# Kernel optimization log

Hardware: AMD Instinct MI355X
Metric: run time of the kernel (lower is better)

Reference implementation:

```python
import jax, jax.numpy as jnp
import numpy as np

IN_F = 4096
OUT_F = 4096
THRESH = 0.1

def setup_inputs() -> dict:
    key = jax.random.key(0)
    kx, kw = jax.random.split(key)
    x = jax.random.normal(kx, (4, 2048, IN_F), dtype=jnp.float32)
    weight = jax.random.normal(kw, (OUT_F, IN_F), dtype=jnp.float32) * 0.5
    bias = jnp.zeros((OUT_F,), dtype=jnp.float32)
    return {"x": x, "weight": weight, "bias": bias}

def reference(x, weight, bias):
    # ternary quantization: sign(w) where |w| > 0.1, else 0
    q = jnp.sign(weight) * (jnp.abs(weight) > THRESH).astype(weight.dtype)
    # straight-through estimator: forward uses q, gradient flows to weight
    w_ste = weight + jax.lax.stop_gradient(q - weight)
    # F.linear: x @ w_ste.T + bias
    return jnp.einsum('bsi,oi->bso', x, w_ste) + bias
```

## Files before the change

### kernel.cpp

```cpp
#include <hip/hip_runtime.h>
#include <cstdint>
#include <cstddef>

#define MDIM 8192
#define NDIM 4096
#define KDIM 4096
#define TERN_THRESH 0.1f

typedef unsigned short u16;
typedef __bf16 bf16x8 __attribute__((ext_vector_type(8)));
typedef float f32x4 __attribute__((ext_vector_type(4)));
typedef u16 u16x8 __attribute__((ext_vector_type(8)));


__device__ __forceinline__ u16 f2bf(float f) {
  unsigned u = __float_as_uint(f);
  u += 0x7FFFu + ((u >> 16) & 1u);
  return (u16)(u >> 16);
}

__device__ __forceinline__ u16 tern_bf16(float w) {
  return w > TERN_THRESH ? (u16)0x3F80u : (w < -TERN_THRESH ? (u16)0xBF80u : (u16)0u);
}

__device__ __forceinline__ void load_lds16(const u16* g, u16* s) {
  __builtin_amdgcn_global_load_lds(
      (__attribute__((address_space(1))) void*)(void*)(g),
      (__attribute__((address_space(3))) void*)(void*)(s),
      16, 0, 0);
}


#define XBLOCKS ((MDIM * (size_t)KDIM) / (8 * 256))
#define WBLOCKS ((NDIM * (size_t)KDIM) / (8 * 256))

__global__ __launch_bounds__(256) void cvt_kernel(const float* __restrict__ x,
                                                  u16* __restrict__ xb,
                                                  const float* __restrict__ w,
                                                  u16* __restrict__ qb) {
  size_t b = blockIdx.x;
  if (b < XBLOCKS) {
    size_t i = b * 256 + threadIdx.x;
    const f32x4* x4 = (const f32x4*)x;
    f32x4 a = __builtin_nontemporal_load(&x4[2 * i]);
    f32x4 c = __builtin_nontemporal_load(&x4[2 * i + 1]);
    u16x8 o;
    o[0] = f2bf(a[0]); o[1] = f2bf(a[1]); o[2] = f2bf(a[2]); o[3] = f2bf(a[3]);
    o[4] = f2bf(c[0]); o[5] = f2bf(c[1]); o[6] = f2bf(c[2]); o[7] = f2bf(c[3]);
    ((u16x8*)xb)[i] = o;
  } else {
    size_t i = (b - XBLOCKS) * 256 + threadIdx.x;
    const f32x4* w4 = (const f32x4*)w;
    f32x4 a = __builtin_nontemporal_load(&w4[2 * i]);
    f32x4 c = __builtin_nontemporal_load(&w4[2 * i + 1]);
    u16x8 o;
    o[0] = tern_bf16(a[0]); o[1] = tern_bf16(a[1]); o[2] = tern_bf16(a[2]); o[3] = tern_bf16(a[3]);
    o[4] = tern_bf16(c[0]); o[5] = tern_bf16(c[1]); o[6] = tern_bf16(c[2]); o[7] = tern_bf16(c[3]);
    ((u16x8*)qb)[i] = o;
  }
}


#define NTILE (KDIM / 32)

#define BARRIER() __builtin_amdgcn_s_barrier()
#define FENCE()   asm volatile("" ::: "memory")
#define VMCNT8()  asm volatile("s_waitcnt vmcnt(8)" ::: "memory")

#define MFMA_BLK(I0)                                                         \
  do {                                                                       \
    _Pragma("unroll") for (int _i = 0; _i < 4; ++_i) {                       \
      _Pragma("unroll") for (int _j = 0; _j < 4; ++_j) {                     \
        acc[(I0) + _i][_j] = __builtin_amdgcn_mfma_f32_16x16x32_bf16(        \
            af[_i], bf[_j], acc[(I0) + _i][_j], 0, 0, 0);                    \
      }                                                                      \
    }                                                                        \
  } while (0)

__global__ __launch_bounds__(512, 2) void gemm_tern_kernel(
    const u16* __restrict__ Xb,
    const u16* __restrict__ Qb,
    const float* __restrict__ bias,
    float* __restrict__ C) {
  __shared__ __attribute__((aligned(16))) u16 As[4 * 8192];
  __shared__ __attribute__((aligned(16))) u16 Bs[4 * 8192];

  const int tid  = threadIdx.x;
  const int lane = tid & 63;
  const int wv   = tid >> 6;
  const int wm   = wv >> 2;
  const int wn   = wv & 3;
  const int quad = lane >> 4;
  const int l16  = lane & 15;

  const int orig    = blockIdx.y * 16 + blockIdx.x;
  const int wg      = (orig & 7) * 64 + (orig >> 3);
  const int rowBase = (wg >> 4) * 256;
  const int colBase = (wg & 15) * 256;

  const u16* gA[2];
  const u16* gB[2];
  int sOff[2];
#pragma unroll
  for (int j = 0; j < 2; ++j) {
    int c  = j * 512 + tid;
    int r  = c >> 2;
    int qg = (c & 3) ^ ((r >> 1) & 3);
    gA[j]   = Xb + (size_t)(rowBase + r) * KDIM + qg * 8;
    gB[j]   = Qb + (size_t)(colBase + r) * KDIM + qg * 8;
    sOff[j] = c * 8;
  }

#define STAGE_A(s, kt)                                              \
  do {                                                              \
    load_lds16(gA[0] + (kt), (u16*)As + (s) * 8192 + sOff[0]);      \
    load_lds16(gA[1] + (kt), (u16*)As + (s) * 8192 + sOff[1]);      \
  } while (0)
#define STAGE_B(s, kt)                                              \
  do {                                                              \
    load_lds16(gB[0] + (kt), (u16*)Bs + (s) * 8192 + sOff[0]);      \
    load_lds16(gB[1] + (kt), (u16*)Bs + (s) * 8192 + sOff[1]);      \
  } while (0)

  int ac[8], bc[4];
#pragma unroll
  for (int i = 0; i < 8; ++i) {
    int r = wm * 128 + i * 16 + l16;
    ac[i] = (r * 4 + (quad ^ ((r >> 1) & 3))) * 8;
  }
#pragma unroll
  for (int j = 0; j < 4; ++j) {
    int r = wn * 64 + j * 16 + l16;
    bc[j] = (r * 4 + (quad ^ ((r >> 1) & 3))) * 8;
  }

#define RD_A(d, i, s) d = *(const bf16x8*)((const u16*)As + (s) * 8192 + ac[i])
#define RD_B(d, j, s) d = *(const bf16x8*)((const u16*)Bs + (s) * 8192 + bc[j])

  f32x4 acc[8][4] = {};
  bf16x8 af[4], bf[4];

  STAGE_A(0, 0);  STAGE_B(0, 0);
  STAGE_A(1, 32); STAGE_B(1, 32);
  STAGE_A(2, 64); STAGE_B(2, 64);
  VMCNT8();
  FENCE(); BARRIER(); FENCE();

#define TILE_BODY(S)                                                       \
  do {                                                                     \
    const int kt = (t + 3 < NTILE) ? (t + 3) * 32 : 0;                     \
                                         \
    RD_A(af[0], 0, S); RD_A(af[1], 1, S);                                  \
    RD_A(af[2], 2, S); RD_A(af[3], 3, S);                                  \
    RD_B(bf[0], 0, S); RD_B(bf[1], 1, S);                                  \
    RD_B(bf[2], 2, S); RD_B(bf[3], 3, S);                                  \
    STAGE_A(((S) + 3) & 3, kt);                                            \
    FENCE(); BARRIER(); FENCE();                                           \
    __builtin_amdgcn_s_setprio(1);                                         \
    MFMA_BLK(0);                                                           \
    __builtin_amdgcn_s_setprio(0);                                         \
    FENCE(); BARRIER(); FENCE();                                           \
                                         \
    RD_A(af[0], 4, S); RD_A(af[1], 5, S);                                  \
    RD_A(af[2], 6, S); RD_A(af[3], 7, S);                                  \
    STAGE_B(((S) + 3) & 3, kt);                                            \
    FENCE(); BARRIER(); FENCE();                                           \
    __builtin_amdgcn_s_setprio(1);                                         \
    MFMA_BLK(4);                                                           \
    __builtin_amdgcn_s_setprio(0);                                         \
    VMCNT8();                                                              \
    FENCE(); BARRIER(); FENCE();                                           \
  } while (0)

  int t = 0;
  for (int it = 0; it < NTILE / 4; ++it) {
    TILE_BODY(0); ++t;
    TILE_BODY(1); ++t;
    TILE_BODY(2); ++t;
    TILE_BODY(3); ++t;
  }

  float bv[4];
#pragma unroll
  for (int j = 0; j < 4; ++j) bv[j] = bias[colBase + wn * 64 + j * 16 + l16];

#pragma unroll
  for (int i = 0; i < 8; ++i) {
#pragma unroll
    for (int r = 0; r < 4; ++r) {
      int grow = rowBase + wm * 128 + i * 16 + quad * 4 + r;
      float* crow = C + (size_t)grow * NDIM + colBase + wn * 64 + l16;
#pragma unroll
      for (int j = 0; j < 4; ++j) {
        crow[j * 16] = acc[i][j][r] + bv[j];
      }
    }
  }
}


extern "C" void kernel_launch(void* const* d_in, const int* in_sizes, int n_in,
                              void* d_out, int out_size, void* d_ws, size_t ws_size,
                              hipStream_t stream) {
  const float* x    = (const float*)d_in[0];
  const float* w    = (const float*)d_in[1];
  const float* bias = (const float*)d_in[2];
  float* out = (float*)d_out;

  u16* xb = (u16*)d_ws;
  u16* qb = xb + (size_t)MDIM * KDIM;

  cvt_kernel<<<(unsigned)(XBLOCKS + WBLOCKS), 256, 0, stream>>>(x, xb, w, qb);

  dim3 grid(NDIM / 256, MDIM / 256);
  gemm_tern_kernel<<<grid, 512, 0, stream>>>(xb, qb, bias, out);
}
```

Baseline: 457.0 us.

## Double-buffer MFMA fragments in registers and cut GEMM barriers to one per tile

```diff
diff --git a/kernel.cpp b/kernel.cpp
--- a/kernel.cpp
+++ b/kernel.cpp
@@ -10,6 +10,7 @@
 typedef unsigned short u16;
 typedef __bf16 bf16x8 __attribute__((ext_vector_type(8)));
 typedef float f32x4 __attribute__((ext_vector_type(4)));
+typedef u16 u16x4 __attribute__((ext_vector_type(4)));
 typedef u16 u16x8 __attribute__((ext_vector_type(8)));
 
 
@@ -40,23 +41,27 @@
                                                   u16* __restrict__ qb) {
   size_t b = blockIdx.x;
   if (b < XBLOCKS) {
-    size_t i = b * 256 + threadIdx.x;
+    size_t i0 = b * 512 + threadIdx.x;
+    size_t i1 = i0 + 256;
     const f32x4* x4 = (const f32x4*)x;
-    f32x4 a = __builtin_nontemporal_load(&x4[2 * i]);
-    f32x4 c = __builtin_nontemporal_load(&x4[2 * i + 1]);
-    u16x8 o;
-    o[0] = f2bf(a[0]); o[1] = f2bf(a[1]); o[2] = f2bf(a[2]); o[3] = f2bf(a[3]);
-    o[4] = f2bf(c[0]); o[5] = f2bf(c[1]); o[6] = f2bf(c[2]); o[7] = f2bf(c[3]);
-    ((u16x8*)xb)[i] = o;
+    f32x4 a = __builtin_nontemporal_load(&x4[i0]);
+    f32x4 c = __builtin_nontemporal_load(&x4[i1]);
+    u16x4 oa, oc;
+    oa[0] = f2bf(a[0]); oa[1] = f2bf(a[1]); oa[2] = f2bf(a[2]); oa[3] = f2bf(a[3]);
+    oc[0] = f2bf(c[0]); oc[1] = f2bf(c[1]); oc[2] = f2bf(c[2]); oc[3] = f2bf(c[3]);
+    ((u16x4*)xb)[i0] = oa;
+    ((u16x4*)xb)[i1] = oc;
   } else {
-    size_t i = (b - XBLOCKS) * 256 + threadIdx.x;
+    size_t i0 = (b - XBLOCKS) * 512 + threadIdx.x;
+    size_t i1 = i0 + 256;
     const f32x4* w4 = (const f32x4*)w;
-    f32x4 a = __builtin_nontemporal_load(&w4[2 * i]);
-    f32x4 c = __builtin_nontemporal_load(&w4[2 * i + 1]);
-    u16x8 o;
-    o[0] = tern_bf16(a[0]); o[1] = tern_bf16(a[1]); o[2] = tern_bf16(a[2]); o[3] = tern_bf16(a[3]);
-    o[4] = tern_bf16(c[0]); o[5] = tern_bf16(c[1]); o[6] = tern_bf16(c[2]); o[7] = tern_bf16(c[3]);
-    ((u16x8*)qb)[i] = o;
+    f32x4 a = __builtin_nontemporal_load(&w4[i0]);
+    f32x4 c = __builtin_nontemporal_load(&w4[i1]);
+    u16x4 oa, oc;
+    oa[0] = tern_bf16(a[0]); oa[1] = tern_bf16(a[1]); oa[2] = tern_bf16(a[2]); oa[3] = tern_bf16(a[3]);
+    oc[0] = tern_bf16(c[0]); oc[1] = tern_bf16(c[1]); oc[2] = tern_bf16(c[2]); oc[3] = tern_bf16(c[3]);
+    ((u16x4*)qb)[i0] = oa;
+    ((u16x4*)qb)[i1] = oc;
   }
 }
 
@@ -65,14 +70,14 @@
 
 #define BARRIER() __builtin_amdgcn_s_barrier()
 #define FENCE()   asm volatile("" ::: "memory")
-#define VMCNT8()  asm volatile("s_waitcnt vmcnt(8)" ::: "memory")
-
-#define MFMA_BLK(I0)                                                         \
+#define VMCNT4()  asm volatile("s_waitcnt vmcnt(4)" ::: "memory")
+
+#define MFMA16(AF, BF, I0)                                                   \
   do {                                                                       \
     _Pragma("unroll") for (int _i = 0; _i < 4; ++_i) {                       \
       _Pragma("unroll") for (int _j = 0; _j < 4; ++_j) {                     \
         acc[(I0) + _i][_j] = __builtin_amdgcn_mfma_f32_16x16x32_bf16(        \
-            af[_i], bf[_j], acc[(I0) + _i][_j], 0, 0, 0);                    \
+            AF[_i], BF[_j], acc[(I0) + _i][_j], 0, 0, 0);                    \
       }                                                                      \
     }                                                                        \
   } while (0)
@@ -138,47 +143,51 @@
 #define RD_B(d, j, s) d = *(const bf16x8*)((const u16*)Bs + (s) * 8192 + bc[j])
 
   f32x4 acc[8][4] = {};
-  bf16x8 af[4], bf[4];
+  bf16x8 a0[4], b0[4], a1[4], b1[4], ab[4];
 
   STAGE_A(0, 0);  STAGE_B(0, 0);
   STAGE_A(1, 32); STAGE_B(1, 32);
   STAGE_A(2, 64); STAGE_B(2, 64);
-  VMCNT8();
+  VMCNT4();
   FENCE(); BARRIER(); FENCE();
-
-#define TILE_BODY(S)                                                       \
+  RD_A(a0[0], 0, 0); RD_A(a0[1], 1, 0); RD_A(a0[2], 2, 0); RD_A(a0[3], 3, 0);
+  RD_B(b0[0], 0, 0); RD_B(b0[1], 1, 0); RD_B(b0[2], 2, 0); RD_B(b0[3], 3, 0);
+
+#define TILE(S, AC, BC, AN, BN, PRE)                                       \
   do {                                                                     \
     const int kt = (t + 3 < NTILE) ? (t + 3) * 32 : 0;                     \
-                                         \
-    RD_A(af[0], 0, S); RD_A(af[1], 1, S);                                  \
-    RD_A(af[2], 2, S); RD_A(af[3], 3, S);                                  \
-    RD_B(bf[0], 0, S); RD_B(bf[1], 1, S);                                  \
-    RD_B(bf[2], 2, S); RD_B(bf[3], 3, S);                                  \
+    RD_A(ab[0], 4, S); RD_A(ab[1], 5, S);                                  \
+    RD_A(ab[2], 6, S); RD_A(ab[3], 7, S);                                  \
     STAGE_A(((S) + 3) & 3, kt);                                            \
+    __builtin_amdgcn_s_setprio(1);                                         \
+    MFMA16(AC, BC, 0);                                                     \
+    __builtin_amdgcn_s_setprio(0);                                         \
+    if (PRE) {                                                             \
+      RD_A(AN[0], 0, ((S) + 1) & 3); RD_A(AN[1], 1, ((S) + 1) & 3);        \
+      RD_A(AN[2], 2, ((S) + 1) & 3); RD_A(AN[3], 3, ((S) + 1) & 3);        \
+      RD_B(BN[0], 0, ((S) + 1) & 3); RD_B(BN[1], 1, ((S) + 1) & 3);        \
+      RD_B(BN[2], 2, ((S) + 1) & 3); RD_B(BN[3], 3, ((S) + 1) & 3);        \
+    }                                                                      \
+    STAGE_B(((S) + 3) & 3, kt);                                            \
+    __builtin_amdgcn_s_setprio(1);                                         \
+    MFMA16(ab, BC, 4);                                                     \
+    __builtin_amdgcn_s_setprio(0);                                         \
+    VMCNT4();                                                              \
     FENCE(); BARRIER(); FENCE();                                           \
-    __builtin_amdgcn_s_setprio(1);                                         \
-    MFMA_BLK(0);                                                           \
-    __builtin_amdgcn_s_setprio(0);                                         \
-    FENCE(); BARRIER(); FENCE();                                           \
-                                         \
-    RD_A(af[0], 4, S); RD_A(af[1], 5, S);                                  \
-    RD_A(af[2], 6, S); RD_A(af[3], 7, S);                                  \
-    STAGE_B(((S) + 3) & 3, kt);                                            \
-    FENCE(); BARRIER(); FENCE();                                           \
-    __builtin_amdgcn_s_setprio(1);                                         \
-    MFMA_BLK(4);                                                           \
-    __builtin_amdgcn_s_setprio(0);                                         \
-    VMCNT8();                                                              \
-    FENCE(); BARRIER(); FENCE();                                           \
+    ++t;                                                                   \
   } while (0)
 
   int t = 0;
-  for (int it = 0; it < NTILE / 4; ++it) {
-    TILE_BODY(0); ++t;
-    TILE_BODY(1); ++t;
-    TILE_BODY(2); ++t;
-    TILE_BODY(3); ++t;
-  }
+  for (int it = 0; it < NTILE / 4 - 1; ++it) {
+    TILE(0, a0, b0, a1, b1, 1);
+    TILE(1, a1, b1, a0, b0, 1);
+    TILE(2, a0, b0, a1, b1, 1);
+    TILE(3, a1, b1, a0, b0, 1);
+  }
+  TILE(0, a0, b0, a1, b1, 1);
+  TILE(1, a1, b1, a0, b0, 1);
+  TILE(2, a0, b0, a1, b1, 1);
+  TILE(3, a1, b1, a0, b0, 0);
 
   float bv[4];
 #pragma unroll
```

Measured after the change: 460.9 us. About the same (+0.9%).
